# Kernel tuning notes

Hardware: AMD Instinct MI355X
Metric: run time of the kernel (lower is better)

Reference implementation:

```python
import jax, jax.numpy as jnp
import numpy as np

INPUT, HIDDEN, OUTPUT = 512, 1024, 512
BATCH, SEQ = 64, 512


def setup_inputs() -> dict:
    key = jax.random.key(0)
    ks = jax.random.split(key, 16)
    s_in = 1.0 / np.sqrt(INPUT)
    s_h = 1.0 / np.sqrt(HIDDEN)
    d = {
        'x': jax.random.normal(ks[0], (BATCH, SEQ, INPUT), jnp.float32),
        'Wxf': jax.random.uniform(ks[1], (HIDDEN, INPUT), jnp.float32, -s_in, s_in),
        'Whf': jax.random.uniform(ks[2], (HIDDEN, HIDDEN), jnp.float32, -s_h, s_h),
        'bhf': jax.random.uniform(ks[3], (HIDDEN,), jnp.float32, -s_h, s_h),
        'Wxi': jax.random.uniform(ks[4], (HIDDEN, INPUT), jnp.float32, -s_in, s_in),
        'Whi': jax.random.uniform(ks[5], (HIDDEN, HIDDEN), jnp.float32, -s_h, s_h),
        'bhi': jax.random.uniform(ks[6], (HIDDEN,), jnp.float32, -s_h, s_h),
        'Wxc': jax.random.uniform(ks[7], (HIDDEN, INPUT), jnp.float32, -s_in, s_in),
        'Whc': jax.random.uniform(ks[8], (HIDDEN, HIDDEN), jnp.float32, -s_h, s_h),
        'bhc': jax.random.uniform(ks[9], (HIDDEN,), jnp.float32, -s_h, s_h),
        'Wxo': jax.random.uniform(ks[10], (HIDDEN, INPUT), jnp.float32, -s_in, s_in),
        'Who': jax.random.uniform(ks[11], (HIDDEN, HIDDEN), jnp.float32, -s_h, s_h),
        'bho': jax.random.uniform(ks[12], (HIDDEN,), jnp.float32, -s_h, s_h),
        'Wout': jax.random.uniform(ks[13], (OUTPUT, HIDDEN), jnp.float32, -s_h, s_h),
        'bout': jax.random.uniform(ks[14], (OUTPUT,), jnp.float32, -s_h, s_h),
    }
    return d


def _lstm(x, Wxf, Whf, bhf, Wxi, Whi, bhi, Wxc, Whc, bhc, Wxo, Who, bho, Wout, bout):
    B = x.shape[0]
    H = Whf.shape[0]
    # Precompute input-to-gate projections for all timesteps in one big GEMM.
    Wx = jnp.concatenate([Wxf, Wxi, Wxc, Wxo], axis=0)          # (4H, I)
    gx = jnp.einsum('bti,gi->tbg', x, Wx)                        # (T, B, 4H)
    Wh = jnp.concatenate([Whf, Whi, Whc, Who], axis=0)          # (4H, H)
    bh = jnp.concatenate([bhf, bhi, bhc, bho], axis=0)          # (4H,)

    def step(carry, gxt):
        h, c = carry
        g = gxt + h @ Wh.T + bh                                  # (B, 4H)
        f = jax.nn.sigmoid(g[:, 0 * H:1 * H])
        i = jax.nn.sigmoid(g[:, 1 * H:2 * H])
        chat = jnp.tanh(g[:, 2 * H:3 * H])
        o = jax.nn.sigmoid(g[:, 3 * H:4 * H])
        c = f * c + i * chat
        h = o * jnp.tanh(c)
        return (h, c), None

    h0 = jnp.zeros((B, H), x.dtype)
    c0 = jnp.zeros((B, H), x.dtype)
    (h, _), _ = jax.lax.scan(step, (h0, c0), gx)
    return h @ Wout.T + bout                                     # (B, OUTPUT)


def reference(x, Wxf, Whf, bhf, Wxi, Whi, bhi, Wxc, Whc, bhc, Wxo, Who, bho, Wout, bout):
    return _lstm(x, Wxf, Whf, bhf, Wxi, Whi, bhi, Wxc, Whc, bhc, Wxo, Who, bho, Wout, bout)
```

## Files before the change

### kernel.cpp

```cpp
#include <hip/hip_runtime.h>

#define T_SEQ 512
#define NBATCH 64
#define NIN 512
#define NHID 1024
#define NOUT 512
#define KTOT 1536
#define NBLK_R 256
#define NDOM 4
#define UBLK 64

typedef __bf16 bf16;
typedef unsigned long long u64;
typedef __attribute__((ext_vector_type(8))) __bf16 bf16x8;
typedef __attribute__((ext_vector_type(4))) float f32x4;

#define OFF_XB   0ull
#define OFF_W    33554432ull
#define OFF_WOUT 46137344ull
#define OFF_H    47185920ull
#define OFF_FLAG 114425856ull
#define WS_NEEDED (OFF_FLAG + 513ull * NDOM * UBLK * 4)

#define MFMA16(a, b, c) __builtin_amdgcn_mfma_f32_16x16x32_bf16(a, b, c, 0, 0, 0)


__global__ void pack_weights(const float* __restrict__ Wxf, const float* __restrict__ Whf,
                             const float* __restrict__ Wxi, const float* __restrict__ Whi,
                             const float* __restrict__ Wxc, const float* __restrict__ Whc,
                             const float* __restrict__ Wxo, const float* __restrict__ Who,
                             const float* __restrict__ Wout,
                             bf16* __restrict__ Wcat, bf16* __restrict__ Woutb) {
    int r = blockIdx.x;
    if (r < 4 * NHID) {
        int g = r >> 10, j = r & (NHID - 1);
        const float* Wx = (g == 0 ? Wxf : g == 1 ? Wxi : g == 2 ? Wxc : Wxo);
        const float* Wh = (g == 0 ? Whf : g == 1 ? Whi : g == 2 ? Whc : Who);
        for (int k = threadIdx.x; k < KTOT; k += blockDim.x) {
            float v = (k < NIN) ? Wx[(size_t)j * NIN + k] : Wh[(size_t)j * NHID + (k - NIN)];
            Wcat[(size_t)r * KTOT + k] = (bf16)v;
        }
    } else {
        int o = r - 4 * NHID;
        for (int k = threadIdx.x; k < NHID; k += blockDim.x)
            Woutb[(size_t)o * NHID + k] = (bf16)Wout[(size_t)o * NHID + k];
    }
}

__global__ void conv_x(const float* __restrict__ x, bf16* __restrict__ xb) {
    int bt = blockIdx.x;
    int b = bt >> 9, t = bt & (T_SEQ - 1);
    const float* src = x + ((size_t)b * T_SEQ + t) * NIN;
    bf16* dst = xb + ((size_t)t * NBATCH + b) * NIN;
    for (int i = threadIdx.x; i < NIN; i += blockDim.x)
        dst[i] = (bf16)src[i];
}

__global__ void zero_init(unsigned int* __restrict__ flags, unsigned int* __restrict__ h0) {
    const int n_fl = 513 * NDOM * UBLK;
    const int n_h0 = NDOM * 16384 / 2;
    for (int i = blockIdx.x * blockDim.x + threadIdx.x; i < n_fl; i += gridDim.x * blockDim.x)
        flags[i] = 0;
    for (int i = blockIdx.x * blockDim.x + threadIdx.x; i < n_h0; i += gridDim.x * blockDim.x)
        h0[i] = 0;
}

__launch_bounds__(256, 1)
__global__ void lstm_rec(const bf16* __restrict__ xb, const bf16* __restrict__ Wcat,
                         const float* __restrict__ bhf, const float* __restrict__ bhi,
                         const float* __restrict__ bhc, const float* __restrict__ bho,
                         bf16* __restrict__ hs, unsigned int* __restrict__ flags) {
    const int blk = blockIdx.x;
    const int bg = blk & (NDOM - 1);
    const int ub = blk >> 2;
    const int tid = threadIdx.x;
    const int g = tid >> 6;
    const int l = tid & 63;
    const int col = l & 15;
    const int khalf = l >> 4;

    __shared__ float part[4][16][18];
    __shared__ u64 hstage[64];

    bf16x8 br[48];
    {
        const bf16* wrow = Wcat + ((size_t)(g * NHID + ub * 16 + col)) * KTOT + khalf * 8;
#pragma unroll
        for (int s = 0; s < 48; ++s) br[s] = *(const bf16x8*)(wrow + s * 32);
    }

    const int eu = tid >> 4;
    const int eb = tid & 15;
    const float b_f = bhf[ub * 16 + eu];
    const float b_i = bhi[ub * 16 + eu];
    const float b_c = bhc[ub * 16 + eu];
    const float b_o = bho[ub * 16 + eu];
    float c_state = 0.f;

    const int ug0 = khalf >> 1;
    const int uo = (khalf & 1) * 8;

    for (int t = 0; t < T_SEQ; ++t) {
        f32x4 acc0 = {0.f, 0.f, 0.f, 0.f}, acc1 = acc0;

        const bf16* ax = xb + ((size_t)t * NBATCH + bg * 16 + col) * NIN + khalf * 8;
#pragma unroll
        for (int s = 0; s < 16; s += 2) {
            acc0 = MFMA16(*(const bf16x8*)(ax + s * 32), br[s], acc0);
            acc1 = MFMA16(*(const bf16x8*)(ax + (s + 1) * 32), br[s + 1], acc1);
        }

        if (t > 0) {
            if (tid < 64) {
                const unsigned int* fl = flags + ((size_t)t * NDOM + bg) * UBLK;
                while (__hip_atomic_load(&fl[l], __ATOMIC_RELAXED,
                                         __HIP_MEMORY_SCOPE_AGENT) != 1u) {}
            }
            __syncthreads();
            __builtin_amdgcn_fence(__ATOMIC_ACQUIRE, "workgroup");
        }

        const bf16* hpl = hs + ((size_t)t * NDOM + bg) * 16384;
#pragma unroll
        for (int s = 16; s < 48; s += 2) {
            int ugA = (s - 16) * 2 + ug0;
            int ugB = (s - 15) * 2 + ug0;
            acc0 = MFMA16(*(const bf16x8*)(hpl + ugA * 256 + col * 16 + uo), br[s], acc0);
            acc1 = MFMA16(*(const bf16x8*)(hpl + ugB * 256 + col * 16 + uo), br[s + 1], acc1);
        }

#pragma unroll
        for (int r = 0; r < 4; ++r)
            part[g][khalf * 4 + r][col] = acc0[r] + acc1[r];
        __syncthreads();

        float gf = part[0][eb][eu] + b_f;
        float gi = part[1][eb][eu] + b_i;
        float gc = part[2][eb][eu] + b_c;
        float go = part[3][eb][eu] + b_o;
        float f  = 1.f / (1.f + __expf(-gf));
        float ii = 1.f / (1.f + __expf(-gi));
        float ch = 1.f - 2.f / (__expf(2.f * gc) + 1.f);
        float o  = 1.f / (1.f + __expf(-go));
        c_state = f * c_state + ii * ch;
        float th = 1.f - 2.f / (__expf(2.f * c_state) + 1.f);
        ((bf16*)hstage)[eb * 16 + eu] = (bf16)(o * th);
        __syncthreads();

        if (tid < 64) {
            u64* dst = (u64*)(hs + ((size_t)(t + 1) * NDOM + bg) * 16384) + ub * 64 + tid;
            __hip_atomic_store(dst, hstage[tid], __ATOMIC_RELAXED, __HIP_MEMORY_SCOPE_AGENT);
        }
        __syncthreads();
        if (tid == 0)
            __hip_atomic_store(&flags[((size_t)(t + 1) * NDOM + bg) * UBLK + ub], 1u,
                               __ATOMIC_RELEASE, __HIP_MEMORY_SCOPE_AGENT);
    }
}

__launch_bounds__(256)
__global__ void out_gemm(const bf16* __restrict__ hs, const bf16* __restrict__ Woutb,
                         const float* __restrict__ bout, float* __restrict__ out) {
    int blk = blockIdx.x;
    int tid = threadIdx.x;
    int w = tid >> 6, l = tid & 63, col = l & 15, khalf = l >> 4;
    int oc = blk * 16 + col;
    const bf16* hpl = hs + ((size_t)T_SEQ * NDOM + w) * 16384;
    const bf16* bp = Woutb + (size_t)oc * NHID + khalf * 8;
    const int ug0 = khalf >> 1, uo = (khalf & 1) * 8;
    f32x4 acc = {0.f, 0.f, 0.f, 0.f};
#pragma unroll
    for (int ks = 0; ks < 32; ++ks) {
        bf16x8 a = *(const bf16x8*)(hpl + (ks * 2 + ug0) * 256 + col * 16 + uo);
        bf16x8 b = *(const bf16x8*)(bp + ks * 32);
        acc = MFMA16(a, b, acc);
    }
    float bo = bout[oc];
#pragma unroll
    for (int r = 0; r < 4; ++r) {
        int b = w * 16 + khalf * 4 + r;
        out[(size_t)b * NOUT + oc] = acc[r] + bo;
    }
}

extern "C" void kernel_launch(void* const* d_in, const int* in_sizes, int n_in,
                              void* d_out, int out_size, void* d_ws, size_t ws_size,
                              hipStream_t stream) {
    const float* x    = (const float*)d_in[0];
    const float* Wxf  = (const float*)d_in[1];
    const float* Whf  = (const float*)d_in[2];
    const float* bhf  = (const float*)d_in[3];
    const float* Wxi  = (const float*)d_in[4];
    const float* Whi  = (const float*)d_in[5];
    const float* bhi  = (const float*)d_in[6];
    const float* Wxc  = (const float*)d_in[7];
    const float* Whc  = (const float*)d_in[8];
    const float* bhc  = (const float*)d_in[9];
    const float* Wxo  = (const float*)d_in[10];
    const float* Who  = (const float*)d_in[11];
    const float* bho  = (const float*)d_in[12];
    const float* Wout = (const float*)d_in[13];
    const float* bout = (const float*)d_in[14];

    if (ws_size < WS_NEEDED) return;

    char* ws = (char*)d_ws;
    bf16* xb    = (bf16*)(ws + OFF_XB);
    bf16* Wcat  = (bf16*)(ws + OFF_W);
    bf16* Woutb = (bf16*)(ws + OFF_WOUT);
    bf16* hs    = (bf16*)(ws + OFF_H);
    unsigned int* flags = (unsigned int*)(ws + OFF_FLAG);

    pack_weights<<<4 * NHID + NOUT, 256, 0, stream>>>(Wxf, Whf, Wxi, Whi, Wxc, Whc,
                                                      Wxo, Who, Wout, Wcat, Woutb);
    conv_x<<<T_SEQ * NBATCH, 256, 0, stream>>>(x, xb);
    zero_init<<<256, 256, 0, stream>>>(flags, (unsigned int*)hs);
    lstm_rec<<<NBLK_R, 256, 0, stream>>>(xb, Wcat, bhf, bhi, bhc, bho, hs, flags);
    out_gemm<<<NOUT / 16, 256, 0, stream>>>(hs, Woutb, bout, (float*)d_out);
}
```

Before: 3.888 ms.

## Stage x and h tiles in LDS via async loads, split K across waves

```diff
diff --git a/kernel.cpp b/kernel.cpp
--- a/kernel.cpp
+++ b/kernel.cpp
@@ -23,6 +23,25 @@
 #define WS_NEEDED (OFF_FLAG + 513ull * NDOM * UBLK * 4)
 
 #define MFMA16(a, b, c) __builtin_amdgcn_mfma_f32_16x16x32_bf16(a, b, c, 0, 0, 0)
+
+#define XLDS0  0
+#define XLDS1  16384
+#define HLDS   32768
+#define PART   65536
+#define HSTAGE 82944
+#define LDS_SZ 83456
+
+#define WAITVM(N) do { asm volatile("s_waitcnt vmcnt(" #N ")" ::: "memory"); \
+                       __builtin_amdgcn_sched_barrier(0); } while (0)
+#define WAITLG    do { asm volatile("s_waitcnt lgkmcnt(0)" ::: "memory"); \
+                       __builtin_amdgcn_sched_barrier(0); } while (0)
+#define BAR()     __builtin_amdgcn_s_barrier()
+
+__device__ __forceinline__ void glds16(const void* g, void* l) {
+    __builtin_amdgcn_global_load_lds(
+        (const __attribute__((address_space(1))) void*)g,
+        (__attribute__((address_space(3))) void*)l, 16, 0, 0);
+}
 
 
 __global__ void pack_weights(const float* __restrict__ Wxf, const float* __restrict__ Whf,
@@ -51,9 +70,9 @@
     int bt = blockIdx.x;
     int b = bt >> 9, t = bt & (T_SEQ - 1);
     const float* src = x + ((size_t)b * T_SEQ + t) * NIN;
-    bf16* dst = xb + ((size_t)t * NBATCH + b) * NIN;
-    for (int i = threadIdx.x; i < NIN; i += blockDim.x)
-        dst[i] = (bf16)src[i];
+    bf16* dst = xb + ((size_t)t * NDOM + (b >> 4)) * 8192 + (b & 15) * 16;
+    for (int k = threadIdx.x; k < NIN; k += blockDim.x)
+        dst[(k >> 4) * 256 + (k & 15)] = (bf16)src[k];
 }
 
 __global__ void zero_init(unsigned int* __restrict__ flags, unsigned int* __restrict__ h0) {
@@ -70,91 +89,137 @@
                          const float* __restrict__ bhf, const float* __restrict__ bhi,
                          const float* __restrict__ bhc, const float* __restrict__ bho,
                          bf16* __restrict__ hs, unsigned int* __restrict__ flags) {
+    __shared__ __attribute__((aligned(128))) char smem[LDS_SZ];
+
     const int blk = blockIdx.x;
     const int bg = blk & (NDOM - 1);
     const int ub = blk >> 2;
     const int tid = threadIdx.x;
-    const int g = tid >> 6;
+    const int w = tid >> 6;
     const int l = tid & 63;
     const int col = l & 15;
     const int khalf = l >> 4;
 
-    __shared__ float part[4][16][18];
-    __shared__ u64 hstage[64];
-
-    bf16x8 br[48];
-    {
-        const bf16* wrow = Wcat + ((size_t)(g * NHID + ub * 16 + col)) * KTOT + khalf * 8;
-#pragma unroll
-        for (int s = 0; s < 48; ++s) br[s] = *(const bf16x8*)(wrow + s * 32);
-    }
-
-    const int eu = tid >> 4;
-    const int eb = tid & 15;
+    const char* xbB = (const char*)xb;
+    const char* hsB = (const char*)hs;
+
+    bf16x8 br0[12], br1[12], br2[12], br3[12];
+#pragma unroll
+    for (int i = 0; i < 12; ++i) {
+        size_t ko = (size_t)(w + 4 * i) * 32 + khalf * 8;
+        br0[i] = *(const bf16x8*)(Wcat + (size_t)(0 * NHID + ub * 16 + col) * KTOT + ko);
+        br1[i] = *(const bf16x8*)(Wcat + (size_t)(1 * NHID + ub * 16 + col) * KTOT + ko);
+        br2[i] = *(const bf16x8*)(Wcat + (size_t)(2 * NHID + ub * 16 + col) * KTOT + ko);
+        br3[i] = *(const bf16x8*)(Wcat + (size_t)(3 * NHID + ub * 16 + col) * KTOT + ko);
+    }
+
+    const int eb = tid & 15, eu = tid >> 4;
     const float b_f = bhf[ub * 16 + eu];
     const float b_i = bhi[ub * 16 + eu];
     const float b_c = bhc[ub * 16 + eu];
     const float b_o = bho[ub * 16 + eu];
     float c_state = 0.f;
 
-    const int ug0 = khalf >> 1;
-    const int uo = (khalf & 1) * 8;
+    const int a_lane = col * 32 + (khalf & 1) * 16;
+    const int kh2 = khalf >> 1;
+
+    {
+        const char* xt0 = xbB + (size_t)bg * 16384;
+#pragma unroll
+        for (int j = 0; j < 4; ++j)
+            glds16(xt0 + (w * 4 + j) * 1024 + l * 16, smem + XLDS0 + (w * 4 + j) * 1024);
+        WAITVM(0);
+        BAR();
+    }
 
     for (int t = 0; t < T_SEQ; ++t) {
-        f32x4 acc0 = {0.f, 0.f, 0.f, 0.f}, acc1 = acc0;
-
-        const bf16* ax = xb + ((size_t)t * NBATCH + bg * 16 + col) * NIN + khalf * 8;
-#pragma unroll
-        for (int s = 0; s < 16; s += 2) {
-            acc0 = MFMA16(*(const bf16x8*)(ax + s * 32), br[s], acc0);
-            acc1 = MFMA16(*(const bf16x8*)(ax + (s + 1) * 32), br[s + 1], acc1);
-        }
-
-        if (t > 0) {
-            if (tid < 64) {
-                const unsigned int* fl = flags + ((size_t)t * NDOM + bg) * UBLK;
-                while (__hip_atomic_load(&fl[l], __ATOMIC_RELAXED,
-                                         __HIP_MEMORY_SCOPE_AGENT) != 1u) {}
+        if (t > 0 && tid < 64) {
+            const unsigned int* fl = flags + ((size_t)t * NDOM + bg) * UBLK;
+            while (__hip_atomic_load(&fl[l], __ATOMIC_RELAXED,
+                                     __HIP_MEMORY_SCOPE_AGENT) != 1u) {}
+        }
+        BAR();
+
+        const char* hplB = hsB + ((size_t)t * NDOM + bg) * 32768;
+#pragma unroll
+        for (int j = 0; j < 8; ++j)
+            glds16(hplB + (w * 8 + j) * 1024 + l * 16, smem + HLDS + (w * 8 + j) * 1024);
+        WAITVM(8);
+        BAR();
+
+        f32x4 acc0 = {0.f, 0.f, 0.f, 0.f}, acc1 = acc0, acc2 = acc0, acc3 = acc0;
+        const char* xcur = smem + ((t & 1) ? XLDS1 : XLDS0);
+#pragma unroll
+        for (int i = 0; i < 4; ++i) {
+            int ks = w + 4 * i;
+            bf16x8 a = *(const bf16x8*)(xcur + (2 * ks + kh2) * 512 + a_lane);
+            acc0 = MFMA16(a, br0[i], acc0);
+            acc1 = MFMA16(a, br1[i], acc1);
+            acc2 = MFMA16(a, br2[i], acc2);
+            acc3 = MFMA16(a, br3[i], acc3);
+        }
+
+        {
+            int tn = (t + 1 < T_SEQ) ? t + 1 : T_SEQ - 1;
+            const char* xnB = xbB + ((size_t)tn * NDOM + bg) * 16384;
+            char* xnx = smem + ((t & 1) ? XLDS0 : XLDS1);
+#pragma unroll
+            for (int j = 0; j < 4; ++j)
+                glds16(xnB + (w * 4 + j) * 1024 + l * 16, xnx + (w * 4 + j) * 1024);
+        }
+        WAITVM(4);
+        BAR();
+
+#pragma unroll
+        for (int i = 4; i < 12; ++i) {
+            int ks = w + 4 * i;
+            bf16x8 a = *(const bf16x8*)(smem + HLDS + (2 * (ks - 16) + kh2) * 512 + a_lane);
+            acc0 = MFMA16(a, br0[i], acc0);
+            acc1 = MFMA16(a, br1[i], acc1);
+            acc2 = MFMA16(a, br2[i], acc2);
+            acc3 = MFMA16(a, br3[i], acc3);
+        }
+
+        {
+            char* pw = smem + PART + ((w * 4 * 16 + col) * 17 + khalf * 4) * 4;
+            *(f32x4*)(pw + (0 * 16 * 17) * 4) = acc0;
+            *(f32x4*)(pw + (1 * 16 * 17) * 4) = acc1;
+            *(f32x4*)(pw + (2 * 16 * 17) * 4) = acc2;
+            *(f32x4*)(pw + (3 * 16 * 17) * 4) = acc3;
+        }
+        WAITLG;
+        BAR();
+
+        {
+            float gf = b_f, gi = b_i, gc = b_c, go = b_o;
+#pragma unroll
+            for (int w2 = 0; w2 < 4; ++w2) {
+                const char* pb = smem + PART + (((w2 * 4) * 16 + eu) * 17 + eb) * 4;
+                gf += *(const float*)(pb + (0 * 16 * 17) * 4);
+                gi += *(const float*)(pb + (1 * 16 * 17) * 4);
+                gc += *(const float*)(pb + (2 * 16 * 17) * 4);
+                go += *(const float*)(pb + (3 * 16 * 17) * 4);
             }
-            __syncthreads();
-            __builtin_amdgcn_fence(__ATOMIC_ACQUIRE, "workgroup");
-        }
-
-        const bf16* hpl = hs + ((size_t)t * NDOM + bg) * 16384;
-#pragma unroll
-        for (int s = 16; s < 48; s += 2) {
-            int ugA = (s - 16) * 2 + ug0;
-            int ugB = (s - 15) * 2 + ug0;
-            acc0 = MFMA16(*(const bf16x8*)(hpl + ugA * 256 + col * 16 + uo), br[s], acc0);
-            acc1 = MFMA16(*(const bf16x8*)(hpl + ugB * 256 + col * 16 + uo), br[s + 1], acc1);
-        }
-
-#pragma unroll
-        for (int r = 0; r < 4; ++r)
-            part[g][khalf * 4 + r][col] = acc0[r] + acc1[r];
-        __syncthreads();
-
-        float gf = part[0][eb][eu] + b_f;
-        float gi = part[1][eb][eu] + b_i;
-        float gc = part[2][eb][eu] + b_c;
-        float go = part[3][eb][eu] + b_o;
-        float f  = 1.f / (1.f + __expf(-gf));
-        float ii = 1.f / (1.f + __expf(-gi));
-        float ch = 1.f - 2.f / (__expf(2.f * gc) + 1.f);
-        float o  = 1.f / (1.f + __expf(-go));
-        c_state = f * c_state + ii * ch;
-        float th = 1.f - 2.f / (__expf(2.f * c_state) + 1.f);
-        ((bf16*)hstage)[eb * 16 + eu] = (bf16)(o * th);
-        __syncthreads();
+            float f  = 1.f / (1.f + __expf(-gf));
+            float ii = 1.f / (1.f + __expf(-gi));
+            float ch = 1.f - 2.f / (__expf(2.f * gc) + 1.f);
+            float o  = 1.f / (1.f + __expf(-go));
+            c_state = f * c_state + ii * ch;
+            float th = 1.f - 2.f / (__expf(2.f * c_state) + 1.f);
+            *(bf16*)(smem + HSTAGE + (eb * 16 + eu) * 2) = (bf16)(o * th);
+        }
+        WAITLG;
+        BAR();
 
         if (tid < 64) {
-            u64* dst = (u64*)(hs + ((size_t)(t + 1) * NDOM + bg) * 16384) + ub * 64 + tid;
-            __hip_atomic_store(dst, hstage[tid], __ATOMIC_RELAXED, __HIP_MEMORY_SCOPE_AGENT);
-        }
-        __syncthreads();
-        if (tid == 0)
-            __hip_atomic_store(&flags[((size_t)(t + 1) * NDOM + bg) * UBLK + ub], 1u,
-                               __ATOMIC_RELEASE, __HIP_MEMORY_SCOPE_AGENT);
+            u64 v = *(const u64*)(smem + HSTAGE + tid * 8);
+            u64* dst = (u64*)(hsB + ((size_t)(t + 1) * NDOM + bg) * 32768 + ub * 512) + tid;
+            __hip_atomic_store(dst, v, __ATOMIC_RELAXED, __HIP_MEMORY_SCOPE_AGENT);
+            WAITVM(0);
+            if (tid == 0)
+                __hip_atomic_store(&flags[((size_t)(t + 1) * NDOM + bg) * UBLK + ub], 1u,
+                                   __ATOMIC_RELEASE, __HIP_MEMORY_SCOPE_AGENT);
+        }
     }
 }
 
```

Measured after the change: 3.583 ms. 1.08x faster.
